# Kernel optimization log

Hardware: AMD Instinct MI355X
Metric: run time of the kernel (lower is better)

## Reference

```python
import jax, jax.numpy as jnp
import numpy as np
from jax import lax

LAMBDA_REG = 0.01


def setup_inputs() -> dict:
    key = jax.random.key(0)
    k1, k2 = jax.random.split(key)
    features = jax.random.normal(k1, (8192, 512), dtype=jnp.float32)
    attention_scores = jax.random.uniform(k2, (8192,), dtype=jnp.float32)
    return {"features": features, "attention_scores": attention_scores, "k": 256}


def _kernel_matrix(features, attention_scores, lambda_reg=LAMBDA_REG):
    # L_ij = sqrt(q_i q_j) * <f_i, f_j>/(|f_i||f_j|) + lambda * I
    fn = features / jnp.linalg.norm(features, axis=1, keepdims=True)
    S = fn @ fn.T                                   # [N, N] cosine similarity
    q = attention_scores
    L = jnp.sqrt(q[:, None] * q[None, :]) * S
    N = features.shape[0]
    return L + lambda_reg * jnp.eye(N, dtype=features.dtype)


def _greedy_map(L, k):
    # Fast greedy DPP MAP (Chen et al. 2018): incremental Cholesky.
    # Marginal log-det gain of adding item i to selected set Y is log d_i,
    # where d_i = L_ii - ||c_i||^2 is the Schur complement. argmax over d_i
    # equals argmax over logdet(L_{Y+i}) since logdet(L_{Y+i}) = logdet(L_Y) + log d_i.
    N = L.shape[0]

    def step(carry, t):
        d, cis, mask = carry                         # d:[N], cis:[k,N], mask:[N]
        j = jnp.argmax(jnp.where(mask, d, -jnp.inf))  # first max (matches torch '>' tie-break)
        # e_n = (L[j,n] - sum_t cis[t,j]*cis[t,n]) / sqrt(d_j); unused rows of cis are zero
        e = (L[j] - cis[:, j] @ cis) / jnp.sqrt(d[j])  # [N]
        cis = cis.at[t].set(e)
        return (d - e * e, cis, mask.at[j].set(False)), j

    init = (jnp.diagonal(L), jnp.zeros((k, N), L.dtype), jnp.ones(N, dtype=bool))
    _, idx = lax.scan(step, init, jnp.arange(k))
    return idx                                        # [k] int selected indices


def reference(features, attention_scores, k):
    L = _kernel_matrix(features, attention_scores)
    return _greedy_map(L, k)
```

## Files before the change

### kernel.cpp

```cpp
#include <hip/hip_runtime.h>
#include <math.h>
#include <stdint.h>


#define N 8192
#define D 512
#define K 256
#define LAMBDA_REG 0.01f
#define NBLK 256
#define NTHR 256
#define ROWS 32
#define RS   560
#define CS   68
#define CTS  264
#define SCOPE __HIP_MEMORY_SCOPE_AGENT

typedef unsigned long long u64;
typedef float f32x4 __attribute__((ext_vector_type(4)));

struct __align__(8) Pick { float v; int i; };

__device__ __forceinline__ bool better(float av, int ai, float bv, int bi) {
    return (av > bv) || (av == bv && ai < bi);
}

__device__ __forceinline__ u64 pack_slot(float v, int idx, int tag) {
    unsigned hi = ((unsigned)tag << 13) | (unsigned)idx;
    return ((u64)hi << 32) | (u64)__float_as_uint(v);
}

__device__ __forceinline__ void bypass_store_u64(u64* p, u64 v) {
    asm volatile("global_store_dwordx2 %0, %1, off sc0 sc1"
                 :: "v"(p), "v"(v) : "memory");
}

__device__ __forceinline__ void bypass_store_f32x4(const f32x4* p, f32x4 v) {
    asm volatile("global_store_dwordx4 %0, %1, off sc0 sc1"
                 :: "v"(p), "v"(v) : "memory");
}

__device__ __forceinline__ f32x4 bypass_load_f32x4(const f32x4* p) {
    f32x4 r;
    asm volatile("global_load_dwordx4 %0, %1, off sc0 sc1"
                 : "=v"(r) : "v"(p));
    return r;
}

__global__ __launch_bounds__(NTHR, 1) void dpp_kernel(
        const float* __restrict__ F, const float* __restrict__ q,
        float* __restrict__ FN, float* __restrict__ cisT,
        u64* __restrict__ slots, int* __restrict__ out)
{
    const int tid = threadIdx.x;
    const int blk = blockIdx.x;
    const int r   = tid >> 3;
    const int c   = tid & 7;
    const int n   = blk * ROWS + r;

    __shared__ __align__(16) float lds_fn[ROWS * RS];
    __shared__ __align__(16) float lds_ct[ROWS * CTS];
    __shared__ __align__(16) float lds_gj[8 * CS];
    __shared__ __align__(16) float lds_cj[K];
    __shared__ Pick lds_wave[NTHR / 64];
    __shared__ Pick lds_final;

    const f32x4* F4  = reinterpret_cast<const f32x4*>(F);
    f32x4*       FN4 = reinterpret_cast<f32x4*>(FN);

    float dloc, qn;
    bool  masked = false;
    {
        const f32x4* src = F4 + (size_t)n * (D / 4) + c * 16;
        float* frow = &lds_fn[r * RS + c * CS];
        float ss = 0.f;
        #pragma unroll
        for (int i = 0; i < 16; ++i) {
            f32x4 v = src[i];
            *reinterpret_cast<f32x4*>(frow + 4 * i) = v;
            ss = fmaf(v.x, v.x, ss); ss = fmaf(v.y, v.y, ss);
            ss = fmaf(v.z, v.z, ss); ss = fmaf(v.w, v.w, ss);
        }
        ss += __shfl_xor(ss, 1); ss += __shfl_xor(ss, 2); ss += __shfl_xor(ss, 4);
        const float norm = sqrtf(ss);
        f32x4* dst = FN4 + (size_t)n * (D / 4) + c * 16;
        float ssn = 0.f;
        #pragma unroll
        for (int i = 0; i < 16; ++i) {
            f32x4 v = *reinterpret_cast<f32x4*>(frow + 4 * i);
            v.x /= norm; v.y /= norm; v.z /= norm; v.w /= norm;
            *reinterpret_cast<f32x4*>(frow + 4 * i) = v;
            bypass_store_f32x4(dst + i, v);
            ssn = fmaf(v.x, v.x, ssn); ssn = fmaf(v.y, v.y, ssn);
            ssn = fmaf(v.z, v.z, ssn); ssn = fmaf(v.w, v.w, ssn);
        }
        ssn += __shfl_xor(ssn, 1); ssn += __shfl_xor(ssn, 2); ssn += __shfl_xor(ssn, 4);
        qn = q[n];
        dloc = fmaf(sqrtf(qn * qn), ssn, LAMBDA_REG);
    }

    {
        float v = dloc; int idx = n;
        #pragma unroll
        for (int m = 32; m > 0; m >>= 1) {
            float ov = __shfl_xor(v, m);
            int   oi = __shfl_xor(idx, m);
            if (better(ov, oi, v, idx)) { v = ov; idx = oi; }
        }
        if ((tid & 63) == 0) { lds_wave[tid >> 6].v = v; lds_wave[tid >> 6].i = idx; }
        asm volatile("s_waitcnt vmcnt(0)" ::: "memory");
        __syncthreads();
        if (tid == 0) {
            Pick p = lds_wave[0];
            #pragma unroll
            for (int w = 1; w < NTHR / 64; ++w) {
                Pick o = lds_wave[w];
                if (better(o.v, o.i, p.v, p.i)) p = o;
            }
            bypass_store_u64(&slots[blk], pack_slot(p.v, p.i, 0));
        }
    }

    for (int t = 0; t < K; ++t) {
        if (tid < 64) {
            const u64* pb = slots + (t & 1) * NBLK;
            const int s = tid * 4;
            u64 x0, x1, x2, x3;
            const unsigned want = (unsigned)t;
            while (true) {
                x0 = __hip_atomic_load(pb + s,     __ATOMIC_RELAXED, SCOPE);
                x1 = __hip_atomic_load(pb + s + 1, __ATOMIC_RELAXED, SCOPE);
                x2 = __hip_atomic_load(pb + s + 2, __ATOMIC_RELAXED, SCOPE);
                x3 = __hip_atomic_load(pb + s + 3, __ATOMIC_RELAXED, SCOPE);
                bool ok = ((unsigned)(x0 >> 45) == want) &&
                          ((unsigned)(x1 >> 45) == want) &&
                          ((unsigned)(x2 >> 45) == want) &&
                          ((unsigned)(x3 >> 45) == want);
                if (__all(ok)) break;
                __builtin_amdgcn_s_sleep(1);
            }
            asm volatile("" ::: "memory");
            float v = __uint_as_float((unsigned)x0);
            int idx = (int)((x0 >> 32) & 8191u);
            {
                float w = __uint_as_float((unsigned)x1); int k1 = (int)((x1 >> 32) & 8191u);
                if (better(w, k1, v, idx)) { v = w; idx = k1; }
                w = __uint_as_float((unsigned)x2); k1 = (int)((x2 >> 32) & 8191u);
                if (better(w, k1, v, idx)) { v = w; idx = k1; }
                w = __uint_as_float((unsigned)x3); k1 = (int)((x3 >> 32) & 8191u);
                if (better(w, k1, v, idx)) { v = w; idx = k1; }
            }
            #pragma unroll
            for (int m = 32; m > 0; m >>= 1) {
                float ov = __shfl_xor(v, m);
                int   oi = __shfl_xor(idx, m);
                if (better(ov, oi, v, idx)) { v = ov; idx = oi; }
            }
            if (tid == 0) { lds_final.v = v; lds_final.i = idx; }
        }
        __syncthreads();
        const float dj = lds_final.v;
        const int   j  = lds_final.i;

        if (blk == 0 && tid == 0) out[t] = j;
        if (t == K - 1) break;

        const float sj = sqrtf(dj);
        const float qj = q[j];

        f32x4 gv;
        float cv;
        if (tid < 128) {
            gv = bypass_load_f32x4(FN4 + (size_t)j * (D / 4) + tid);
        }
        if (tid < t) {
            const float* cp = cisT + (size_t)j * K + tid;
            asm volatile("global_load_dword %0, %1, off sc0 sc1"
                         : "=v"(cv) : "v"(cp));
        }
        asm volatile("s_waitcnt vmcnt(0)" ::: "memory");
        __builtin_amdgcn_sched_barrier(0);
        if (tid < 128) {
            *reinterpret_cast<f32x4*>(&lds_gj[(tid >> 4) * CS + (tid & 15) * 4]) = gv;
        }
        if (tid < t) lds_cj[tid] = cv;
        __syncthreads();

        const float* frow = &lds_fn[r * RS + c * CS];
        const float* grow = &lds_gj[c * CS];
        f32x4 a = {0.f, 0.f, 0.f, 0.f};
        #pragma unroll
        for (int i = 0; i < 16; ++i) {
            f32x4 v = *reinterpret_cast<const f32x4*>(frow + 4 * i);
            f32x4 g = *reinterpret_cast<const f32x4*>(grow + 4 * i);
            a.x = fmaf(v.x, g.x, a.x); a.y = fmaf(v.y, g.y, a.y);
            a.z = fmaf(v.z, g.z, a.z); a.w = fmaf(v.w, g.w, a.w);
        }
        float dot = (a.x + a.y) + (a.z + a.w);
        dot += __shfl_xor(dot, 1); dot += __shfl_xor(dot, 2); dot += __shfl_xor(dot, 4);
        float Ljn = sqrtf(qj * qn) * dot;
        if (n == j) Ljn += LAMBDA_REG;

        float cd = 0.f;
        const float* ctrow = &lds_ct[r * CTS];
        for (int tt = c; tt < t; tt += 8)
            cd = fmaf(lds_cj[tt], ctrow[tt], cd);
        cd += __shfl_xor(cd, 1); cd += __shfl_xor(cd, 2); cd += __shfl_xor(cd, 4);

        const float e = (Ljn - cd) / sj;
        if (c == 0) {
            lds_ct[r * CTS + t] = e;
            const float* ep = cisT + (size_t)n * K + t;
            asm volatile("global_store_dword %0, %1, off sc0 sc1"
                         :: "v"(ep), "v"(e) : "memory");
        }
        dloc = fmaf(-e, e, dloc);
        if (n == j) masked = true;

        {
            float v = masked ? -INFINITY : dloc; int idx = n;
            #pragma unroll
            for (int m = 32; m > 0; m >>= 1) {
                float ov = __shfl_xor(v, m);
                int   oi = __shfl_xor(idx, m);
                if (better(ov, oi, v, idx)) { v = ov; idx = oi; }
            }
            if ((tid & 63) == 0) { lds_wave[tid >> 6].v = v; lds_wave[tid >> 6].i = idx; }
        }
        asm volatile("s_waitcnt vmcnt(0)" ::: "memory");
        __syncthreads();
        if (tid == 0) {
            Pick p = lds_wave[0];
            #pragma unroll
            for (int w = 1; w < NTHR / 64; ++w) {
                Pick o = lds_wave[w];
                if (better(o.v, o.i, p.v, p.i)) p = o;
            }
            bypass_store_u64(&slots[((t + 1) & 1) * NBLK + blk],
                             pack_slot(p.v, p.i, t + 1));
        }
    }
}

extern "C" void kernel_launch(void* const* d_in, const int* in_sizes, int n_in,
                              void* d_out, int out_size, void* d_ws, size_t ws_size,
                              hipStream_t stream) {
    const float* F = (const float*)d_in[0];
    const float* q = (const float*)d_in[1];
    int* out = (int*)d_out;

    uint8_t* w = (uint8_t*)d_ws;
    u64*   slots = (u64*)(w + 256);
    float* FN    = (float*)(w + 8192);
    float* cisT  = (float*)(w + 8192 + (size_t)N * D * 4);

    hipMemsetAsync((void*)(w + 256), 0xFF, 4096, stream);
    hipLaunchKernelGGL(dpp_kernel, dim3(NBLK), dim3(NTHR), 0, stream,
                       F, q, FN, cisT, slots, out);
}
```

Baseline: 1.370 ms.

## Replace all-to-all argmax polling with a two-level relay reduction

Previously every block polled all 256 per-block argmax slots each iteration. Now 8 relay blocks each reduce a group of 32 slots and publish one partial winner, and every block polls only those 8 relay entries. This cuts global polling traffic and contention on the slots at the cost of an extra publish/poll hop on the critical path of each step. The cache-bypassing asm loads for the selected feature row and its cisT column are also replaced with ordinary loads. That lets the compiler schedule them, but it risks reading stale data written by blocks on other XCDs.

After: 1.289 ms. 5.9% less time.

```diff
diff --git a/kernel.cpp b/kernel.cpp
--- a/kernel.cpp
+++ b/kernel.cpp
@@ -13,6 +13,8 @@
 #define RS   560
 #define CS   68
 #define CTS  264
+#define NRELAY 8
+#define GRP  32
 #define SCOPE __HIP_MEMORY_SCOPE_AGENT
 
 typedef unsigned long long u64;
@@ -39,23 +41,18 @@
                  :: "v"(p), "v"(v) : "memory");
 }
 
-__device__ __forceinline__ f32x4 bypass_load_f32x4(const f32x4* p) {
-    f32x4 r;
-    asm volatile("global_load_dwordx4 %0, %1, off sc0 sc1"
-                 : "=v"(r) : "v"(p));
-    return r;
-}
-
 __global__ __launch_bounds__(NTHR, 1) void dpp_kernel(
         const float* __restrict__ F, const float* __restrict__ q,
         float* __restrict__ FN, float* __restrict__ cisT,
-        u64* __restrict__ slots, int* __restrict__ out)
+        u64* __restrict__ slots, u64* __restrict__ relay,
+        int* __restrict__ out)
 {
     const int tid = threadIdx.x;
     const int blk = blockIdx.x;
     const int r   = tid >> 3;
     const int c   = tid & 7;
     const int n   = blk * ROWS + r;
+    const bool isRelay = (blk < NRELAY);
 
     __shared__ __align__(16) float lds_fn[ROWS * RS];
     __shared__ __align__(16) float lds_ct[ROWS * CTS];
@@ -121,40 +118,50 @@
     }
 
     for (int t = 0; t < K; ++t) {
-        if (tid < 64) {
-            const u64* pb = slots + (t & 1) * NBLK;
-            const int s = tid * 4;
-            u64 x0, x1, x2, x3;
-            const unsigned want = (unsigned)t;
+        const unsigned want = (unsigned)t;
+
+        if (isRelay && tid < 64) {
+            const u64* pb = slots + (t & 1) * NBLK + blk * GRP;
+            u64 x = 0;
             while (true) {
-                x0 = __hip_atomic_load(pb + s,     __ATOMIC_RELAXED, SCOPE);
-                x1 = __hip_atomic_load(pb + s + 1, __ATOMIC_RELAXED, SCOPE);
-                x2 = __hip_atomic_load(pb + s + 2, __ATOMIC_RELAXED, SCOPE);
-                x3 = __hip_atomic_load(pb + s + 3, __ATOMIC_RELAXED, SCOPE);
-                bool ok = ((unsigned)(x0 >> 45) == want) &&
-                          ((unsigned)(x1 >> 45) == want) &&
-                          ((unsigned)(x2 >> 45) == want) &&
-                          ((unsigned)(x3 >> 45) == want);
+                if (tid < GRP) x = __hip_atomic_load(pb + tid, __ATOMIC_RELAXED, SCOPE);
+                bool ok = (tid >= GRP) || ((unsigned)(x >> 45) == want);
                 if (__all(ok)) break;
                 __builtin_amdgcn_s_sleep(1);
             }
             asm volatile("" ::: "memory");
-            float v = __uint_as_float((unsigned)x0);
-            int idx = (int)((x0 >> 32) & 8191u);
-            {
-                float w = __uint_as_float((unsigned)x1); int k1 = (int)((x1 >> 32) & 8191u);
-                if (better(w, k1, v, idx)) { v = w; idx = k1; }
-                w = __uint_as_float((unsigned)x2); k1 = (int)((x2 >> 32) & 8191u);
-                if (better(w, k1, v, idx)) { v = w; idx = k1; }
-                w = __uint_as_float((unsigned)x3); k1 = (int)((x3 >> 32) & 8191u);
-                if (better(w, k1, v, idx)) { v = w; idx = k1; }
-            }
+            float v = (tid < GRP) ? __uint_as_float((unsigned)x) : -INFINITY;
+            int idx = (tid < GRP) ? (int)((x >> 32) & 8191u) : 0x7fffffff;
             #pragma unroll
             for (int m = 32; m > 0; m >>= 1) {
                 float ov = __shfl_xor(v, m);
                 int   oi = __shfl_xor(idx, m);
                 if (better(ov, oi, v, idx)) { v = ov; idx = oi; }
             }
+            if (tid == 0)
+                bypass_store_u64(&relay[(t & 1) * (NRELAY * 8) + blk * 8],
+                                 pack_slot(v, idx, t));
+        }
+
+        if (tid < 64) {
+            const u64* rb = relay + (t & 1) * (NRELAY * 8);
+            u64 x = 0;
+            while (true) {
+                if (tid < NRELAY)
+                    x = __hip_atomic_load(rb + tid * 8, __ATOMIC_RELAXED, SCOPE);
+                bool ok = (tid >= NRELAY) || ((unsigned)(x >> 45) == want);
+                if (__all(ok)) break;
+                __builtin_amdgcn_s_sleep(1);
+            }
+            asm volatile("" ::: "memory");
+            float v = (tid < NRELAY) ? __uint_as_float((unsigned)x) : -INFINITY;
+            int idx = (tid < NRELAY) ? (int)((x >> 32) & 8191u) : 0x7fffffff;
+            #pragma unroll
+            for (int m = 32; m > 0; m >>= 1) {
+                float ov = __shfl_xor(v, m);
+                int   oi = __shfl_xor(idx, m);
+                if (better(ov, oi, v, idx)) { v = ov; idx = oi; }
+            }
             if (tid == 0) { lds_final.v = v; lds_final.i = idx; }
         }
         __syncthreads();
@@ -169,20 +176,11 @@
 
         f32x4 gv;
         float cv;
-        if (tid < 128) {
-            gv = bypass_load_f32x4(FN4 + (size_t)j * (D / 4) + tid);
-        }
-        if (tid < t) {
-            const float* cp = cisT + (size_t)j * K + tid;
-            asm volatile("global_load_dword %0, %1, off sc0 sc1"
-                         : "=v"(cv) : "v"(cp));
-        }
-        asm volatile("s_waitcnt vmcnt(0)" ::: "memory");
-        __builtin_amdgcn_sched_barrier(0);
-        if (tid < 128) {
+        if (tid < 128) gv = FN4[(size_t)j * (D / 4) + tid];
+        if (tid < t)   cv = cisT[(size_t)j * K + tid];
+        if (tid < 128)
             *reinterpret_cast<f32x4*>(&lds_gj[(tid >> 4) * CS + (tid & 15) * 4]) = gv;
-        }
-        if (tid < t) lds_cj[tid] = cv;
+        if (tid < t)   lds_cj[tid] = cv;
         __syncthreads();
 
         const float* frow = &lds_fn[r * RS + c * CS];
@@ -249,11 +247,12 @@
     int* out = (int*)d_out;
 
     uint8_t* w = (uint8_t*)d_ws;
-    u64*   slots = (u64*)(w + 256);
-    float* FN    = (float*)(w + 8192);
-    float* cisT  = (float*)(w + 8192 + (size_t)N * D * 4);
-
-    hipMemsetAsync((void*)(w + 256), 0xFF, 4096, stream);
+    u64*   slots = (u64*)(w + 1024);
+    u64*   relay = (u64*)(w + 8192);
+    float* FN    = (float*)(w + 16384);
+    float* cisT  = (float*)(w + 16384 + (size_t)N * D * 4);
+
+    hipMemsetAsync((void*)w, 0xFF, 16384, stream);
     hipLaunchKernelGGL(dpp_kernel, dim3(NBLK), dim3(NTHR), 0, stream,
-                       F, q, FN, cisT, slots, out);
-}
+                       F, q, FN, cisT, slots, relay, out);
+}
```

## Centralize grid argmax reduction in block 0 and broadcast via padded mailboxes

Applied to the files above, without the earlier changes.

Before, all 256 blocks each polled every block's slot to reduce the global argmax. Now only block 0 polls and reduces the slots, then writes the winner into a per-block mailbox that each other block polls with a single thread. Slots and mailboxes are padded to 64-byte strides to avoid false sharing, and the FN row and cisT gathers switch from cache-bypassing asm loads to plain loads. This cuts global polling traffic and contention, but it adds a second cross-block hop per step. The plain loads also risk reading stale cached data written by other blocks.

After: 1.286 ms. 1.07x faster.

```diff
diff --git a/kernel.cpp b/kernel.cpp
--- a/kernel.cpp
+++ b/kernel.cpp
@@ -13,6 +13,7 @@
 #define RS   560
 #define CS   68
 #define CTS  264
+#define SSTR 8
 #define SCOPE __HIP_MEMORY_SCOPE_AGENT
 
 typedef unsigned long long u64;
@@ -39,17 +40,11 @@
                  :: "v"(p), "v"(v) : "memory");
 }
 
-__device__ __forceinline__ f32x4 bypass_load_f32x4(const f32x4* p) {
-    f32x4 r;
-    asm volatile("global_load_dwordx4 %0, %1, off sc0 sc1"
-                 : "=v"(r) : "v"(p));
-    return r;
-}
-
 __global__ __launch_bounds__(NTHR, 1) void dpp_kernel(
         const float* __restrict__ F, const float* __restrict__ q,
         float* __restrict__ FN, float* __restrict__ cisT,
-        u64* __restrict__ slots, int* __restrict__ out)
+        u64* __restrict__ slots, u64* __restrict__ mbox,
+        int* __restrict__ out)
 {
     const int tid = threadIdx.x;
     const int blk = blockIdx.x;
@@ -116,46 +111,67 @@
                 Pick o = lds_wave[w];
                 if (better(o.v, o.i, p.v, p.i)) p = o;
             }
-            bypass_store_u64(&slots[blk], pack_slot(p.v, p.i, 0));
+            bypass_store_u64(&slots[blk * SSTR], pack_slot(p.v, p.i, 0));
         }
     }
 
     for (int t = 0; t < K; ++t) {
-        if (tid < 64) {
-            const u64* pb = slots + (t & 1) * NBLK;
-            const int s = tid * 4;
-            u64 x0, x1, x2, x3;
-            const unsigned want = (unsigned)t;
-            while (true) {
-                x0 = __hip_atomic_load(pb + s,     __ATOMIC_RELAXED, SCOPE);
-                x1 = __hip_atomic_load(pb + s + 1, __ATOMIC_RELAXED, SCOPE);
-                x2 = __hip_atomic_load(pb + s + 2, __ATOMIC_RELAXED, SCOPE);
-                x3 = __hip_atomic_load(pb + s + 3, __ATOMIC_RELAXED, SCOPE);
-                bool ok = ((unsigned)(x0 >> 45) == want) &&
-                          ((unsigned)(x1 >> 45) == want) &&
-                          ((unsigned)(x2 >> 45) == want) &&
-                          ((unsigned)(x3 >> 45) == want);
-                if (__all(ok)) break;
-                __builtin_amdgcn_s_sleep(1);
-            }
-            asm volatile("" ::: "memory");
-            float v = __uint_as_float((unsigned)x0);
-            int idx = (int)((x0 >> 32) & 8191u);
-            {
-                float w = __uint_as_float((unsigned)x1); int k1 = (int)((x1 >> 32) & 8191u);
-                if (better(w, k1, v, idx)) { v = w; idx = k1; }
-                w = __uint_as_float((unsigned)x2); k1 = (int)((x2 >> 32) & 8191u);
-                if (better(w, k1, v, idx)) { v = w; idx = k1; }
-                w = __uint_as_float((unsigned)x3); k1 = (int)((x3 >> 32) & 8191u);
-                if (better(w, k1, v, idx)) { v = w; idx = k1; }
-            }
-            #pragma unroll
-            for (int m = 32; m > 0; m >>= 1) {
-                float ov = __shfl_xor(v, m);
-                int   oi = __shfl_xor(idx, m);
-                if (better(ov, oi, v, idx)) { v = ov; idx = oi; }
-            }
-            if (tid == 0) { lds_final.v = v; lds_final.i = idx; }
+        const unsigned want = (unsigned)t;
+
+        if (blk == 0) {
+            if (tid < 64) {
+                const u64* pb = slots + (t & 1) * NBLK * SSTR;
+                u64 x0, x1, x2, x3;
+                while (true) {
+                    x0 = __hip_atomic_load(pb + (tid * 4 + 0) * SSTR, __ATOMIC_RELAXED, SCOPE);
+                    x1 = __hip_atomic_load(pb + (tid * 4 + 1) * SSTR, __ATOMIC_RELAXED, SCOPE);
+                    x2 = __hip_atomic_load(pb + (tid * 4 + 2) * SSTR, __ATOMIC_RELAXED, SCOPE);
+                    x3 = __hip_atomic_load(pb + (tid * 4 + 3) * SSTR, __ATOMIC_RELAXED, SCOPE);
+                    bool ok = ((unsigned)(x0 >> 45) == want) &&
+                              ((unsigned)(x1 >> 45) == want) &&
+                              ((unsigned)(x2 >> 45) == want) &&
+                              ((unsigned)(x3 >> 45) == want);
+                    if (__all(ok)) break;
+                    __builtin_amdgcn_s_sleep(1);
+                }
+                asm volatile("" ::: "memory");
+                float v = __uint_as_float((unsigned)x0);
+                int idx = (int)((x0 >> 32) & 8191u);
+                {
+                    float w = __uint_as_float((unsigned)x1); int k1 = (int)((x1 >> 32) & 8191u);
+                    if (better(w, k1, v, idx)) { v = w; idx = k1; }
+                    w = __uint_as_float((unsigned)x2); k1 = (int)((x2 >> 32) & 8191u);
+                    if (better(w, k1, v, idx)) { v = w; idx = k1; }
+                    w = __uint_as_float((unsigned)x3); k1 = (int)((x3 >> 32) & 8191u);
+                    if (better(w, k1, v, idx)) { v = w; idx = k1; }
+                }
+                #pragma unroll
+                for (int m = 32; m > 0; m >>= 1) {
+                    float ov = __shfl_xor(v, m);
+                    int   oi = __shfl_xor(idx, m);
+                    if (better(ov, oi, v, idx)) { v = ov; idx = oi; }
+                }
+                const u64 msg = pack_slot(v, idx, t);
+                u64* mb = mbox + (t & 1) * NBLK * SSTR;
+                bypass_store_u64(mb + (tid * 4 + 0) * SSTR, msg);
+                bypass_store_u64(mb + (tid * 4 + 1) * SSTR, msg);
+                bypass_store_u64(mb + (tid * 4 + 2) * SSTR, msg);
+                bypass_store_u64(mb + (tid * 4 + 3) * SSTR, msg);
+                if (tid == 0) { lds_final.v = v; lds_final.i = idx; }
+            }
+        } else {
+            if (tid == 0) {
+                const u64* mp = mbox + ((t & 1) * NBLK + blk) * SSTR;
+                u64 x;
+                while (true) {
+                    x = __hip_atomic_load(mp, __ATOMIC_RELAXED, SCOPE);
+                    if ((unsigned)(x >> 45) == want) break;
+                    __builtin_amdgcn_s_sleep(1);
+                }
+                asm volatile("" ::: "memory");
+                lds_final.v = __uint_as_float((unsigned)x);
+                lds_final.i = (int)((x >> 32) & 8191u);
+            }
         }
         __syncthreads();
         const float dj = lds_final.v;
@@ -169,20 +185,11 @@
 
         f32x4 gv;
         float cv;
-        if (tid < 128) {
-            gv = bypass_load_f32x4(FN4 + (size_t)j * (D / 4) + tid);
-        }
-        if (tid < t) {
-            const float* cp = cisT + (size_t)j * K + tid;
-            asm volatile("global_load_dword %0, %1, off sc0 sc1"
-                         : "=v"(cv) : "v"(cp));
-        }
-        asm volatile("s_waitcnt vmcnt(0)" ::: "memory");
-        __builtin_amdgcn_sched_barrier(0);
-        if (tid < 128) {
+        if (tid < 128) gv = FN4[(size_t)j * (D / 4) + tid];
+        if (tid < t)   cv = cisT[(size_t)j * K + tid];
+        if (tid < 128)
             *reinterpret_cast<f32x4*>(&lds_gj[(tid >> 4) * CS + (tid & 15) * 4]) = gv;
-        }
-        if (tid < t) lds_cj[tid] = cv;
+        if (tid < t)   lds_cj[tid] = cv;
         __syncthreads();
 
         const float* frow = &lds_fn[r * RS + c * CS];
@@ -235,7 +242,7 @@
                 Pick o = lds_wave[w];
                 if (better(o.v, o.i, p.v, p.i)) p = o;
             }
-            bypass_store_u64(&slots[((t + 1) & 1) * NBLK + blk],
+            bypass_store_u64(&slots[(((t + 1) & 1) * NBLK + blk) * SSTR],
                              pack_slot(p.v, p.i, t + 1));
         }
     }
@@ -249,11 +256,12 @@
     int* out = (int*)d_out;
 
     uint8_t* w = (uint8_t*)d_ws;
-    u64*   slots = (u64*)(w + 256);
-    float* FN    = (float*)(w + 8192);
-    float* cisT  = (float*)(w + 8192 + (size_t)N * D * 4);
-
-    hipMemsetAsync((void*)(w + 256), 0xFF, 4096, stream);
+    u64*   slots = (u64*)(w + 4096);
+    u64*   mbox  = (u64*)(w + 4096 + 32768);
+    float* FN    = (float*)(w + 131072);
+    float* cisT  = (float*)(w + 131072 + (size_t)N * D * 4);
+
+    hipMemsetAsync((void*)w, 0xFF, 131072, stream);
     hipLaunchKernelGGL(dpp_kernel, dim3(NBLK), dim3(NTHR), 0, stream,
-                       F, q, FN, cisT, slots, out);
-}
+                       F, q, FN, cisT, slots, mbox, out);
+}
```
